# Kernel tuning notes

Measured on AMD Instinct MI355X. Metric: run time of the kernel, lower is better.

The kernel has to match this reference:

```python
import jax, jax.numpy as jnp
import numpy as np

BANDS = [[0,63],[48,111],[96,159],[144,207],[192,255],[240,303],[288,351],[336,399],[384,447],[432,495],[480,543],[528,591],[576,639],[624,687],[672,735],[720,783],[768,831],[816,879],[864,927],[912,975],[960,1023],[961,1024]]
N_FFT, WIN, HOP, FREQ = 2048, 2048, 512, 1025
B, T, D = 8, 2048, 128
NB = len(BANDS)
WIDTH = BANDS[0][1] - BANDS[0][0] + 1  # 64, all bands equal width
STARTS = np.array([s for s, _ in BANDS])
POS = STARTS[:, None] + np.arange(WIDTH)[None, :]  # (NB, WIDTH) freq-bin indices


def setup_inputs() -> dict:
    key = jax.random.key(0)
    k1, k2, k3 = jax.random.split(key, 3)
    z = jax.random.normal(k1, (B, T, NB, D), jnp.float32)
    mix_spec = jax.random.normal(k2, (B, 2, T, FREQ), jnp.float32)
    W = jax.random.normal(k3, (NB, D, WIDTH * 2), jnp.float32) * 1e-4  # init std=0.0001
    b = jnp.zeros((NB, WIDTH * 2), jnp.float32).at[:, 0::2].set(1.0)   # real part bias = 1
    return {"z": z, "mix_spec": mix_spec, "W": W, "b": b}


def _istft(spec_r, spec_i):
    # spec_r/spec_i: (B, T, F) -> waveform (B, HOP*(T-1)), center=True semantics
    comp = spec_r + 1j * spec_i
    frames = jnp.fft.irfft(comp, n=N_FFT, axis=-1)  # (B, T, n_fft)
    n = jnp.arange(WIN, dtype=frames.dtype)
    win = 0.5 * (1.0 - jnp.cos(2.0 * jnp.pi * n / WIN))  # periodic Hann
    frames = frames * win
    total = HOP * (T - 1) + N_FFT
    pos = HOP * jnp.arange(T)[:, None] + jnp.arange(N_FFT)[None, :]  # (T, n_fft)
    out = jnp.zeros((frames.shape[0], total), frames.dtype).at[:, pos].add(frames)
    env = jnp.zeros((total,), frames.dtype).at[pos].add(win * win)
    out = out / jnp.where(env > 1e-11, env, 1.0)
    start = N_FFT // 2
    return out[:, start:start + HOP * (T - 1)]


def reference(z, mix_spec, W, b):
    # per-band linear projections (all same width -> one batched einsum)
    band = jnp.einsum('btnd,ndo->btno', z, W) + b          # (B, T, NB, 2*WIDTH)
    band = band.reshape(B, T, NB, WIDTH, 2)
    # scatter-add into overlapping frequency ranges + overlap-count normalization
    mask = jnp.zeros((B, T, FREQ, 2), z.dtype).at[:, :, POS, :].add(band)
    wgt = jnp.zeros((FREQ,), z.dtype).at[POS].add(1.0)
    mask = mask / jnp.maximum(wgt, 1.0)[None, None, :, None]
    mask_r, mask_i = mask[..., 0], mask[..., 1]            # (B, T, F)
    mix_r, mix_i = mix_spec[:, 0], mix_spec[:, 1]          # (B, T, F)
    out_r = mask_r * mix_r - mask_i * mix_i
    out_i = mask_r * mix_i + mask_i * mix_r
    return _istft(out_r, out_i)
```

## Files before the change

### kernel.cpp

```cpp
#include <hip/hip_runtime.h>

typedef _Float16 f16x8 __attribute__((ext_vector_type(8)));
typedef float f32x4 __attribute__((ext_vector_type(4)));

#define SLOT_DW 2048
#define WT_BYTE_OFF 134217728
#define T_BYTE_OFF  134938624

__global__ __launch_bounds__(256) void k_init(const float* __restrict__ W,
                                              _Float16* __restrict__ Wt,
                                              float2* __restrict__ Tg) {
  int n = blockIdx.x;
  int tid = threadIdx.x;
  if (n == 22) {
    for (int k = tid; k < 1025; k += 256) {
      float sv, cv;
      sincosf((float)k * 3.0679615757712823e-3f, &sv, &cv);
      Tg[k] = make_float2(cv, sv);
    }
    return;
  }
  __shared__ _Float16 L[128 * 130];
  const float* Wn = W + (size_t)n * 16384;
  for (int el = tid; el < 16384; el += 256) {
    int d = el >> 7, o = el & 127;
    L[d * 130 + o] = (_Float16)(Wn[el] * 4096.0f);
  }
  __syncthreads();
  _Float16* Wtn = Wt + (size_t)n * 16384;
  for (int el = tid; el < 16384; el += 256) {
    int o = el >> 7, d = el & 127;
    Wtn[el] = L[d * 130 + o];
  }
}

__global__ __launch_bounds__(256) void kA(const float* __restrict__ z,
                                          const _Float16* __restrict__ Wt,
                                          _Float16* __restrict__ band) {
  int mt = blockIdx.x;
  int n  = blockIdx.y;
  int r0 = mt * 64;
  __shared__ __align__(16) _Float16 As[64 * 136];
  __shared__ __align__(16) _Float16 Bs[128 * 136];
  int tid = threadIdx.x;
  int cg = tid & 15, rg = tid >> 4;

#pragma unroll
  for (int pass = 0; pass < 4; pass++) {
    int row = pass * 16 + rg;
    const float* src = z + ((size_t)(r0 + row) * 22 + n) * 128 + cg * 8;
    float4 v0 = *(const float4*)src;
    float4 v1 = *(const float4*)(src + 4);
    f16x8 h;
    h[0] = (_Float16)v0.x; h[1] = (_Float16)v0.y; h[2] = (_Float16)v0.z; h[3] = (_Float16)v0.w;
    h[4] = (_Float16)v1.x; h[5] = (_Float16)v1.y; h[6] = (_Float16)v1.z; h[7] = (_Float16)v1.w;
    *(f16x8*)&As[row * 136 + cg * 8] = h;
  }
  const _Float16* Wn = Wt + (size_t)n * 16384;
#pragma unroll
  for (int pass = 0; pass < 8; pass++) {
    int o = pass * 16 + rg;
    *(f16x8*)&Bs[o * 136 + cg * 8] = *(const f16x8*)(Wn + o * 128 + cg * 8);
  }
  __syncthreads();

  int lane = tid & 63, wave = tid >> 6;
  int l16 = lane & 15, quad = lane >> 4;
  f32x4 acc[8];
#pragma unroll
  for (int nt = 0; nt < 8; nt++) acc[nt] = (f32x4){0.f, 0.f, 0.f, 0.f};
#pragma unroll
  for (int kb = 0; kb < 4; kb++) {
    f16x8 a = *(const f16x8*)&As[(wave * 16 + l16) * 136 + kb * 32 + quad * 8];
#pragma unroll
    for (int nt = 0; nt < 8; nt++) {
      f16x8 bf = *(const f16x8*)&Bs[(nt * 16 + l16) * 136 + kb * 32 + quad * 8];
      acc[nt] = __builtin_amdgcn_mfma_f32_16x16x32_f16(a, bf, acc[nt], 0, 0, 0);
    }
  }
  __syncthreads();
  const float inv_scale = 1.0f / 4096.0f;
#pragma unroll
  for (int nt = 0; nt < 8; nt++) {
#pragma unroll
    for (int reg = 0; reg < 4; reg++) {
      int row = wave * 16 + quad * 4 + reg;
      As[row * 136 + nt * 16 + l16] = (_Float16)(acc[nt][reg] * inv_scale);
    }
  }
  __syncthreads();
  int row = tid >> 2;
  int c4 = (tid & 3) * 32;
  const _Float16* srcl = &As[row * 136 + c4];
  _Float16* dst = band + (size_t)(r0 + row) * (SLOT_DW * 2) + n * 128 + c4;
  f16x8 v0 = *(const f16x8*)(srcl);
  f16x8 v1 = *(const f16x8*)(srcl + 8);
  f16x8 v2 = *(const f16x8*)(srcl + 16);
  f16x8 v3 = *(const f16x8*)(srcl + 24);
  *(f16x8*)(dst)      = v0;
  *(f16x8*)(dst + 8)  = v1;
  *(f16x8*)(dst + 16) = v2;
  *(f16x8*)(dst + 24) = v3;
}

__global__ __launch_bounds__(256, 6) void kB(const float* __restrict__ mix,
                                             const float* __restrict__ bias,
                                             float* __restrict__ ws) {
  int r = blockIdx.x;
  int b = r >> 11, t = r & 2047;
  __shared__ __align__(16) unsigned char smem[24592];
  float2* Tl   = (float2*)smem;
  float2* bufA = (float2*)(smem + 8200);
  float*  sr   = (float*)(smem + 16392);
  float*  si   = (float*)(smem + 20492);
  float2* bufB = (float2*)(smem + 16392);
  int tid = threadIdx.x;

  const float2* Tg = (const float2*)((const char*)ws + (T_BYTE_OFF - 0) + 0);
  {
    const float2* Tgg = (const float2*)((const char*)ws + T_BYTE_OFF);
    for (int i = tid; i < 1025; i += 256) Tl[i] = Tgg[i];
  }
  (void)Tg;

  const _Float16* bandg = (const _Float16*)(ws + (size_t)r * SLOT_DW);
  const float* mixr = mix + ((size_t)(b * 2) * 2048 + t) * 1025;
  const float* mixi = mix + ((size_t)(b * 2 + 1) * 2048 + t) * 1025;
  for (int f = tid; f < 1025; f += 256) {
    float mr = 0.f, mi = 0.f;
    int wgt = 0;
    int nhi = f / 48; if (nhi > 20) nhi = 20;
    int nlo = (f >= 16) ? (f - 16) / 48 : 0;
    for (int n = nlo; n <= nhi; n++) {
      int idx = n * 128 + 2 * (f - n * 48);
      mr += (float)bandg[idx]     + bias[idx];
      mi += (float)bandg[idx + 1] + bias[idx + 1];
      wgt++;
    }
    if (f >= 961) {
      int idx = 21 * 128 + 2 * (f - 961);
      mr += (float)bandg[idx]     + bias[idx];
      mi += (float)bandg[idx + 1] + bias[idx + 1];
      wgt++;
    }
    float inv = (wgt == 1) ? 1.0f : ((wgt == 2) ? 0.5f : (1.0f / 3.0f));
    mr *= inv; mi *= inv;
    float xr = mixr[f], xi = mixi[f];
    float outr = mr * xr - mi * xi;
    float outi = mr * xi + mi * xr;
    if (f == 0 || f == 1024) outi = 0.0f;
    sr[f] = outr; si[f] = outi;
  }
  __syncthreads();

  for (int k = tid; k < 1024; k += 256) {
    float Xr = sr[k], Xi = si[k];
    float Yr = sr[1024 - k], Yi = -si[1024 - k];
    float Ar = Xr + Yr, Ai = Xi + Yi;
    float Br = Xr - Yr, Bi = Xi - Yi;
    float2 w = Tl[k];
    bufA[k] = make_float2(Ar - (w.x * Bi + w.y * Br), Ai + (w.x * Br - w.y * Bi));
  }
  __syncthreads();

  float2* src = bufA;
  float2* dst = bufB;
  for (int stage = 0; stage < 10; stage++) {
    int m = 1 << stage;
    for (int idx = tid; idx < 512; idx += 256) {
      int jm = idx & ~(m - 1);
      float2 a = src[idx];
      float2 bv = src[idx + 512];
      float2 sum = make_float2(a.x + bv.x, a.y + bv.y);
      float2 dif = make_float2(a.x - bv.x, a.y - bv.y);
      float2 w = Tl[2 * jm];
      float2 o1 = make_float2(w.x * dif.x - w.y * dif.y, w.x * dif.y + w.y * dif.x);
      dst[idx + jm] = sum;
      dst[idx + jm + m] = o1;
    }
    __syncthreads();
    float2* tmp = src; src = dst; dst = tmp;
  }
  float* slot_f = ws + (size_t)r * SLOT_DW;
  const float inv_n = 1.0f / 2048.0f;
  for (int i = tid; i < 2048; i += 256) {
    float2 zc = src[i >> 1];
    float v = (i & 1) ? zc.y : zc.x;
    float c = (i <= 1024) ? Tl[i].x : Tl[2048 - i].x;
    float win = 0.5f * (1.0f - c);
    slot_f[i] = v * inv_n * win;
  }
}

__global__ __launch_bounds__(256) void kC(const float* __restrict__ ws,
                                          float* __restrict__ out) {
  int b = blockIdx.y;
  int p = blockIdx.x * 256 + threadIdx.x;
  int q = p + 1024;
  int t0 = (q - 1536) >> 9; if (t0 < 0) t0 = 0;
  int t1 = q >> 9;          if (t1 > 2047) t1 = 2047;
  float sum = 0.f;
  for (int t = t0; t <= t1; t++) {
    int i = q - (t << 9);
    sum += ws[(size_t)(b * 2048 + t) * SLOT_DW + i];
  }
  float env;
  if (t1 - t0 == 3) {
    env = 1.5f;
  } else {
    env = 0.f;
    for (int t = t0; t <= t1; t++) {
      int i = q - (t << 9);
      float c = cosf((float)i * 3.0679615757712823e-3f);
      float win = 0.5f * (1.0f - c);
      env += win * win;
    }
  }
  out[(size_t)b * 1048064 + p] = sum / (env > 1e-11f ? env : 1.0f);
}

extern "C" void kernel_launch(void* const* d_in, const int* in_sizes, int n_in,
                              void* d_out, int out_size, void* d_ws, size_t ws_size,
                              hipStream_t stream) {
  const float* z    = (const float*)d_in[0];
  const float* mix  = (const float*)d_in[1];
  const float* W    = (const float*)d_in[2];
  const float* bias = (const float*)d_in[3];
  float* out = (float*)d_out;
  _Float16* Wt = (_Float16*)((char*)d_ws + WT_BYTE_OFF);
  float2* Tg = (float2*)((char*)d_ws + T_BYTE_OFF);

  k_init<<<23, 256, 0, stream>>>(W, Wt, Tg);
  kA<<<dim3(256, 22), 256, 0, stream>>>(z, Wt, (_Float16*)d_ws);
  kB<<<16384, 256, 0, stream>>>(mix, bias, (float*)d_ws);
  kC<<<dim3(4094, 8), 256, 0, stream>>>((const float*)d_ws, out);
}
```

Before: 534.1 us.

## Use radix-4 FFT with padded LDS, on-the-fly twiddles, and register-direct MFMA operands

The per-frame inverse FFT kernel changes from ten radix-2 stages to five radix-4 stages, halving the number of barriers and LDS passes. LDS is padded to avoid bank conflicts, and the twiddle table is replaced by fast __sincosf/__cosf. The pre-twiddle step now handles the conjugate-symmetric pairs k and 1024-k together, so one sync disappears. The projection GEMM now loads z and W straight from global memory into MFMA operand registers instead of staging them in LDS. The trade-off is lower-accuracy fast trig and possibly less coalesced operand loads in the GEMM.

```diff
diff --git a/kernel.cpp b/kernel.cpp
--- a/kernel.cpp
+++ b/kernel.cpp
@@ -1,25 +1,17 @@
 #include <hip/hip_runtime.h>
 
 typedef _Float16 f16x8 __attribute__((ext_vector_type(8)));
+typedef _Float16 f16x2 __attribute__((ext_vector_type(2)));
 typedef float f32x4 __attribute__((ext_vector_type(4)));
 
 #define SLOT_DW 2048
 #define WT_BYTE_OFF 134217728
-#define T_BYTE_OFF  134938624
+#define PHYS(i) ((i) + ((i) >> 5))
 
 __global__ __launch_bounds__(256) void k_init(const float* __restrict__ W,
-                                              _Float16* __restrict__ Wt,
-                                              float2* __restrict__ Tg) {
+                                              _Float16* __restrict__ Wt) {
   int n = blockIdx.x;
   int tid = threadIdx.x;
-  if (n == 22) {
-    for (int k = tid; k < 1025; k += 256) {
-      float sv, cv;
-      sincosf((float)k * 3.0679615757712823e-3f, &sv, &cv);
-      Tg[k] = make_float2(cv, sv);
-    }
-    return;
-  }
   __shared__ _Float16 L[128 * 130];
   const float* Wn = W + (size_t)n * 16384;
   for (int el = tid; el < 16384; el += 256) {
@@ -40,58 +32,52 @@
   int mt = blockIdx.x;
   int n  = blockIdx.y;
   int r0 = mt * 64;
-  __shared__ __align__(16) _Float16 As[64 * 136];
-  __shared__ __align__(16) _Float16 Bs[128 * 136];
+  __shared__ __align__(16) _Float16 Cs[64 * 136];
   int tid = threadIdx.x;
-  int cg = tid & 15, rg = tid >> 4;
-
-#pragma unroll
-  for (int pass = 0; pass < 4; pass++) {
-    int row = pass * 16 + rg;
-    const float* src = z + ((size_t)(r0 + row) * 22 + n) * 128 + cg * 8;
-    float4 v0 = *(const float4*)src;
-    float4 v1 = *(const float4*)(src + 4);
-    f16x8 h;
-    h[0] = (_Float16)v0.x; h[1] = (_Float16)v0.y; h[2] = (_Float16)v0.z; h[3] = (_Float16)v0.w;
-    h[4] = (_Float16)v1.x; h[5] = (_Float16)v1.y; h[6] = (_Float16)v1.z; h[7] = (_Float16)v1.w;
-    *(f16x8*)&As[row * 136 + cg * 8] = h;
-  }
-  const _Float16* Wn = Wt + (size_t)n * 16384;
-#pragma unroll
-  for (int pass = 0; pass < 8; pass++) {
-    int o = pass * 16 + rg;
-    *(f16x8*)&Bs[o * 136 + cg * 8] = *(const f16x8*)(Wn + o * 128 + cg * 8);
-  }
-  __syncthreads();
-
   int lane = tid & 63, wave = tid >> 6;
   int l16 = lane & 15, quad = lane >> 4;
-  f32x4 acc[8];
-#pragma unroll
-  for (int nt = 0; nt < 8; nt++) acc[nt] = (f32x4){0.f, 0.f, 0.f, 0.f};
+
+  const _Float16* Wn = Wt + (size_t)n * 16384;
+  f32x4 acc[2][4];
+#pragma unroll
+  for (int c = 0; c < 2; c++)
+#pragma unroll
+    for (int rt = 0; rt < 4; rt++) acc[c][rt] = (f32x4){0.f, 0.f, 0.f, 0.f};
+
 #pragma unroll
   for (int kb = 0; kb < 4; kb++) {
-    f16x8 a = *(const f16x8*)&As[(wave * 16 + l16) * 136 + kb * 32 + quad * 8];
-#pragma unroll
-    for (int nt = 0; nt < 8; nt++) {
-      f16x8 bf = *(const f16x8*)&Bs[(nt * 16 + l16) * 136 + kb * 32 + quad * 8];
-      acc[nt] = __builtin_amdgcn_mfma_f32_16x16x32_f16(a, bf, acc[nt], 0, 0, 0);
-    }
-  }
-  __syncthreads();
+    int ko = kb * 32 + quad * 8;
+    f16x8 b0 = *(const f16x8*)(Wn + (wave * 32 + l16) * 128 + ko);
+    f16x8 b1 = *(const f16x8*)(Wn + (wave * 32 + 16 + l16) * 128 + ko);
+#pragma unroll
+    for (int rt = 0; rt < 4; rt++) {
+      const float* src = z + ((size_t)(r0 + rt * 16 + l16) * 22 + n) * 128 + ko;
+      float4 v0 = *(const float4*)src;
+      float4 v1 = *(const float4*)(src + 4);
+      f16x8 a;
+      a[0] = (_Float16)v0.x; a[1] = (_Float16)v0.y; a[2] = (_Float16)v0.z; a[3] = (_Float16)v0.w;
+      a[4] = (_Float16)v1.x; a[5] = (_Float16)v1.y; a[6] = (_Float16)v1.z; a[7] = (_Float16)v1.w;
+      acc[0][rt] = __builtin_amdgcn_mfma_f32_16x16x32_f16(a, b0, acc[0][rt], 0, 0, 0);
+      acc[1][rt] = __builtin_amdgcn_mfma_f32_16x16x32_f16(a, b1, acc[1][rt], 0, 0, 0);
+    }
+  }
   const float inv_scale = 1.0f / 4096.0f;
 #pragma unroll
-  for (int nt = 0; nt < 8; nt++) {
-#pragma unroll
-    for (int reg = 0; reg < 4; reg++) {
-      int row = wave * 16 + quad * 4 + reg;
-      As[row * 136 + nt * 16 + l16] = (_Float16)(acc[nt][reg] * inv_scale);
+  for (int c = 0; c < 2; c++) {
+    int col = (wave * 2 + c) * 16 + l16;
+#pragma unroll
+    for (int rt = 0; rt < 4; rt++) {
+#pragma unroll
+      for (int reg = 0; reg < 4; reg++) {
+        int row = rt * 16 + quad * 4 + reg;
+        Cs[row * 136 + col] = (_Float16)(acc[c][rt][reg] * inv_scale);
+      }
     }
   }
   __syncthreads();
   int row = tid >> 2;
   int c4 = (tid & 3) * 32;
-  const _Float16* srcl = &As[row * 136 + c4];
+  const _Float16* srcl = &Cs[row * 136 + c4];
   _Float16* dst = band + (size_t)(r0 + row) * (SLOT_DW * 2) + n * 128 + c4;
   f16x8 v0 = *(const f16x8*)(srcl);
   f16x8 v1 = *(const f16x8*)(srcl + 8);
@@ -103,92 +89,106 @@
   *(f16x8*)(dst + 24) = v3;
 }
 
-__global__ __launch_bounds__(256, 6) void kB(const float* __restrict__ mix,
-                                             const float* __restrict__ bias,
-                                             float* __restrict__ ws) {
+__global__ __launch_bounds__(256) void kB(const float* __restrict__ mix,
+                                          const float* __restrict__ bias,
+                                          float* __restrict__ ws) {
   int r = blockIdx.x;
   int b = r >> 11, t = r & 2047;
-  __shared__ __align__(16) unsigned char smem[24592];
-  float2* Tl   = (float2*)smem;
-  float2* bufA = (float2*)(smem + 8200);
-  float*  sr   = (float*)(smem + 16392);
-  float*  si   = (float*)(smem + 20492);
-  float2* bufB = (float2*)(smem + 16392);
+  __shared__ __align__(16) float2 bufA[1056];
+  __shared__ __align__(16) float2 bufB[1056];
   int tid = threadIdx.x;
 
-  const float2* Tg = (const float2*)((const char*)ws + (T_BYTE_OFF - 0) + 0);
-  {
-    const float2* Tgg = (const float2*)((const char*)ws + T_BYTE_OFF);
-    for (int i = tid; i < 1025; i += 256) Tl[i] = Tgg[i];
-  }
-  (void)Tg;
-
   const _Float16* bandg = (const _Float16*)(ws + (size_t)r * SLOT_DW);
+  const float2* bias2 = (const float2*)bias;
   const float* mixr = mix + ((size_t)(b * 2) * 2048 + t) * 1025;
   const float* mixi = mix + ((size_t)(b * 2 + 1) * 2048 + t) * 1025;
-  for (int f = tid; f < 1025; f += 256) {
-    float mr = 0.f, mi = 0.f;
-    int wgt = 0;
-    int nhi = f / 48; if (nhi > 20) nhi = 20;
-    int nlo = (f >= 16) ? (f - 16) / 48 : 0;
-    for (int n = nlo; n <= nhi; n++) {
-      int idx = n * 128 + 2 * (f - n * 48);
-      mr += (float)bandg[idx]     + bias[idx];
-      mi += (float)bandg[idx + 1] + bias[idx + 1];
-      wgt++;
-    }
-    if (f >= 961) {
-      int idx = 21 * 128 + 2 * (f - 961);
-      mr += (float)bandg[idx]     + bias[idx];
-      mi += (float)bandg[idx + 1] + bias[idx + 1];
-      wgt++;
-    }
-    float inv = (wgt == 1) ? 1.0f : ((wgt == 2) ? 0.5f : (1.0f / 3.0f));
-    mr *= inv; mi *= inv;
-    float xr = mixr[f], xi = mixi[f];
-    float outr = mr * xr - mi * xi;
-    float outi = mr * xi + mi * xr;
-    if (f == 0 || f == 1024) outi = 0.0f;
-    sr[f] = outr; si[f] = outi;
-  }
-  __syncthreads();
-
-  for (int k = tid; k < 1024; k += 256) {
-    float Xr = sr[k], Xi = si[k];
-    float Yr = sr[1024 - k], Yi = -si[1024 - k];
-    float Ar = Xr + Yr, Ai = Xi + Yi;
-    float Br = Xr - Yr, Bi = Xi - Yi;
-    float2 w = Tl[k];
-    bufA[k] = make_float2(Ar - (w.x * Bi + w.y * Br), Ai + (w.x * Br - w.y * Bi));
-  }
-  __syncthreads();
+
+  for (int k = tid; k <= 512; k += 256) {
+    float2 X[2];
+#pragma unroll
+    for (int side = 0; side < 2; side++) {
+      int f = side ? (1024 - k) : k;
+      float mr = 0.f, mi = 0.f;
+      int wgt = 0;
+      int nhi = f / 48; if (nhi > 20) nhi = 20;
+      int nlo = (f >= 16) ? (f - 16) / 48 : 0;
+      for (int n = nlo; n <= nhi; n++) {
+        int idx = n * 128 + 2 * (f - n * 48);
+        f16x2 bv = *(const f16x2*)(bandg + idx);
+        float2 bb = bias2[idx >> 1];
+        mr += (float)bv[0] + bb.x;
+        mi += (float)bv[1] + bb.y;
+        wgt++;
+      }
+      if (f >= 961) {
+        int idx = 21 * 128 + 2 * (f - 961);
+        f16x2 bv = *(const f16x2*)(bandg + idx);
+        float2 bb = bias2[idx >> 1];
+        mr += (float)bv[0] + bb.x;
+        mi += (float)bv[1] + bb.y;
+        wgt++;
+      }
+      float inv = (wgt == 1) ? 1.0f : ((wgt == 2) ? 0.5f : (1.0f / 3.0f));
+      mr *= inv; mi *= inv;
+      float xr = mixr[f], xi = mixi[f];
+      float outr = mr * xr - mi * xi;
+      float outi = mr * xi + mi * xr;
+      if (f == 0 || f == 1024) outi = 0.0f;
+      X[side] = make_float2(outr, outi);
+      if (k == 512) { X[1] = X[0]; break; }
+    }
+    float Ar = X[0].x + X[1].x, Ai = X[0].y - X[1].y;
+    float Br = X[0].x - X[1].x, Bi = X[0].y + X[1].y;
+    float sv, cv;
+    __sincosf((float)k * 3.0679615757712823e-3f, &sv, &cv);
+    float s1 = cv * Bi + sv * Br;
+    float s2 = cv * Br - sv * Bi;
+    bufA[PHYS(k & 1023)] = make_float2(Ar - s1, Ai + s2);
+    if (k > 0 && k < 512) bufA[PHYS(1024 - k)] = make_float2(Ar + s1, -Ai + s2);
+  }
 
   float2* src = bufA;
   float2* dst = bufB;
-  for (int stage = 0; stage < 10; stage++) {
-    int m = 1 << stage;
-    for (int idx = tid; idx < 512; idx += 256) {
-      int jm = idx & ~(m - 1);
-      float2 a = src[idx];
-      float2 bv = src[idx + 512];
-      float2 sum = make_float2(a.x + bv.x, a.y + bv.y);
-      float2 dif = make_float2(a.x - bv.x, a.y - bv.y);
-      float2 w = Tl[2 * jm];
-      float2 o1 = make_float2(w.x * dif.x - w.y * dif.y, w.x * dif.y + w.y * dif.x);
-      dst[idx + jm] = sum;
-      dst[idx + jm + m] = o1;
-    }
+#pragma unroll
+  for (int st = 0; st < 5; st++) {
+    const int s = 2 * st;
+    const int m = 1 << s;
     __syncthreads();
+    int q = tid >> s, rr = tid & (m - 1);
+    float2 x0 = src[PHYS(tid)];
+    float2 x1 = src[PHYS(tid + 256)];
+    float2 x2 = src[PHYS(tid + 512)];
+    float2 x3 = src[PHYS(tid + 768)];
+    float ang = (float)(q * m) * 6.135923151542565e-3f;
+    float ws1, wc1;
+    __sincosf(ang, &ws1, &wc1);
+    float wc2 = wc1 * wc1 - ws1 * ws1, ws2 = 2.0f * wc1 * ws1;
+    float wc3 = wc2 * wc1 - ws2 * ws1, ws3 = wc2 * ws1 + ws2 * wc1;
+    float tAr = x0.x + x2.x, tAi = x0.y + x2.y;
+    float tBr = x0.x - x2.x, tBi = x0.y - x2.y;
+    float tCr = x1.x + x3.x, tCi = x1.y + x3.y;
+    float tDr = x1.x - x3.x, tDi = x1.y - x3.y;
+    int base = 4 * q * m + rr;
+    dst[PHYS(base)] = make_float2(tAr + tCr, tAi + tCi);
+    float pr = tBr - tDi, pi = tBi + tDr;
+    dst[PHYS(base + m)] = make_float2(wc1 * pr - ws1 * pi, wc1 * pi + ws1 * pr);
+    float qr = tAr - tCr, qi = tAi - tCi;
+    dst[PHYS(base + 2 * m)] = make_float2(wc2 * qr - ws2 * qi, wc2 * qi + ws2 * qr);
+    float rr2 = tBr + tDi, ri2 = tBi - tDr;
+    dst[PHYS(base + 3 * m)] = make_float2(wc3 * rr2 - ws3 * ri2, wc3 * ri2 + ws3 * rr2);
     float2* tmp = src; src = dst; dst = tmp;
   }
-  float* slot_f = ws + (size_t)r * SLOT_DW;
+  __syncthreads();
+
+  float2* slot2 = (float2*)(ws + (size_t)r * SLOT_DW);
   const float inv_n = 1.0f / 2048.0f;
-  for (int i = tid; i < 2048; i += 256) {
-    float2 zc = src[i >> 1];
-    float v = (i & 1) ? zc.y : zc.x;
-    float c = (i <= 1024) ? Tl[i].x : Tl[2048 - i].x;
-    float win = 0.5f * (1.0f - c);
-    slot_f[i] = v * inv_n * win;
+  for (int j = tid; j < 1024; j += 256) {
+    float2 g = src[PHYS(j)];
+    float c0 = __cosf((float)(2 * j) * 3.0679615757712823e-3f);
+    float c1 = __cosf((float)(2 * j + 1) * 3.0679615757712823e-3f);
+    float w0 = 0.5f * (1.0f - c0);
+    float w1 = 0.5f * (1.0f - c1);
+    slot2[j] = make_float2(g.x * inv_n * w0, g.y * inv_n * w1);
   }
 }
 
@@ -211,7 +211,7 @@
     env = 0.f;
     for (int t = t0; t <= t1; t++) {
       int i = q - (t << 9);
-      float c = cosf((float)i * 3.0679615757712823e-3f);
+      float c = __cosf((float)i * 3.0679615757712823e-3f);
       float win = 0.5f * (1.0f - c);
       env += win * win;
     }
@@ -228,9 +228,8 @@
   const float* bias = (const float*)d_in[3];
   float* out = (float*)d_out;
   _Float16* Wt = (_Float16*)((char*)d_ws + WT_BYTE_OFF);
-  float2* Tg = (float2*)((char*)d_ws + T_BYTE_OFF);
-
-  k_init<<<23, 256, 0, stream>>>(W, Wt, Tg);
+
+  k_init<<<22, 256, 0, stream>>>(W, Wt);
   kA<<<dim3(256, 22), 256, 0, stream>>>(z, Wt, (_Float16*)d_ws);
   kB<<<16384, 256, 0, stream>>>(mix, bias, (float*)d_ws);
   kC<<<dim3(4094, 8), 256, 0, stream>>>((const float*)d_ws, out);
```

Measured after the change: 532.4 us. About the same (-0.3%).
